# Performance work log

Measured on AMD Instinct MI355X. Metric: run time of the kernel, lower is better.

## Reference

```python
import jax, jax.numpy as jnp
import numpy as np

B, T, C = 256, 512, 256
K = 8  # number of distinct phoneme classes used (indices into phoneme_inventory)
# weights dict {'aa':2.0,'ae':0.5,'ah':1.5,'ao':1.2,'aw':0.8}, rest default 1.0,
# materialized as a dense per-class-index weight vector:
WEIGHTS = np.ones(K, dtype=np.float32)
WEIGHTS[:5] = [2.0, 0.5, 1.5, 1.2, 0.8]


def setup_inputs() -> dict:
    key = jax.random.key(0)
    k1, k2 = jax.random.split(key)
    embeddings = jax.random.normal(k1, (B, T, C), dtype=jnp.float32)
    phonemes = jax.random.randint(k2, (B, T), 0, K, dtype=jnp.int64)
    weights = jnp.asarray(WEIGHTS)
    return {"embeddings": embeddings, "phonemes": phonemes, "weights": weights}


def reference(embeddings, phonemes, weights):
    Bs, Ts, Cs = embeddings.shape
    # F.normalize(p=2, dim=-1) with eps=1e-12
    norm = jnp.linalg.norm(embeddings, axis=-1, keepdims=True)
    emb = embeddings / jnp.maximum(norm, 1e-12)
    # all-pairs cosine similarity per timestep: [T, B, B]
    exp_sim = jnp.exp(jnp.einsum('itc,jtc->tij', emb, emb))
    eye = jnp.eye(Bs, dtype=bool)  # [B, B]
    p = phonemes.T  # [T, B]
    pos = (p[:, :, None] == p[:, None, :]) & ~eye  # [T, B, B]
    num = jnp.where(pos, exp_sim, 0.0).sum(-1)          # [T, B]
    den = jnp.where(~eye, exp_sim, 0.0).sum(-1)          # [T, B]
    per_sample = -jnp.log(num / (den + 1e-6))            # [T, B]
    # segment-mean per (timestep, class), then weighted mean over present classes
    oh = jax.nn.one_hot(p, weights.shape[0], dtype=per_sample.dtype)  # [T, B, K]
    counts = oh.sum(1)                                   # [T, K]
    sums = jnp.einsum('tb,tbk->tk', per_sample, oh)      # [T, K]
    present = counts > 0
    class_mean = sums / jnp.maximum(counts, 1.0)
    loss_t = jnp.where(present, class_mean * weights, 0.0).sum(-1) / present.sum(-1)
    return loss_t.mean()
```

## Files before the change

### kernel.cpp

```cpp
#include <hip/hip_runtime.h>

#define Bn 256
#define Tn 512
#define Cn 256
#define Kn 8

typedef __attribute__((ext_vector_type(4))) float f32x4;

__global__ __launch_bounds__(256, 8)
void conv_k(const float* __restrict__ emb, unsigned char* __restrict__ ws) {
    const int gid = blockIdx.x * 256 + threadIdx.x;
    const int b   = gid & 31;
    const int idx = gid >> 5;
    const int row = idx >> 9;
    const int t   = idx & (Tn - 1);
    const float4* p = (const float4*)(emb + (size_t)idx * Cn) + 2 * b;
    const float4 v0 = p[0];
    const float4 v1 = p[1];
    float ss = v0.x*v0.x + v0.y*v0.y + v0.z*v0.z + v0.w*v0.w
             + v1.x*v1.x + v1.y*v1.y + v1.z*v1.z + v1.w*v1.w;
    #pragma unroll
    for (int m = 1; m <= 16; m <<= 1) ss += __shfl_xor(ss, m, 64);
    const float inv = rsqrtf(fmaxf(ss, 1e-24f));
    int lo = __builtin_amdgcn_cvt_pk_fp8_f32(v0.x * inv, v0.y * inv, 0, false);
    lo     = __builtin_amdgcn_cvt_pk_fp8_f32(v0.z * inv, v0.w * inv, lo, true);
    int hi = __builtin_amdgcn_cvt_pk_fp8_f32(v1.x * inv, v1.y * inv, 0, false);
    hi     = __builtin_amdgcn_cvt_pk_fp8_f32(v1.z * inv, v1.w * inv, hi, true);
    const int q = b & 3, kk = b >> 2, kp = kk >> 1;
    const int phys = ((((q << 2) + kp) ^ (row & 7)) << 4) + ((kk & 1) << 3);
    int2 pk; pk.x = lo; pk.y = hi;
    *(int2*)&ws[(size_t)t * 65536 + row * 256 + phys] = pk;
}

__global__ __launch_bounds__(512, 4)
void tcon_k(const unsigned char* __restrict__ ws,
            const int* __restrict__ phon,
            const float* __restrict__ wts,
            float* __restrict__ out) {
    __shared__ __align__(16) unsigned char Esh[Bn * Bn];
    __shared__ int   pcls[Bn];
    __shared__ float num_s[Bn], den_s[Bn];
    __shared__ float csum[Kn];
    __shared__ int   ccnt[Kn];

    const int t    = blockIdx.x;
    const int tid  = threadIdx.x;
    const int lane = tid & 63;
    const int wave = tid >> 6;

    if (tid < Kn) { csum[tid] = 0.0f; ccnt[tid] = 0; }
    if (tid < Bn) pcls[tid] = phon[tid * Tn + t];

    {
        const unsigned char* src = ws + (size_t)t * 65536;
        #pragma unroll
        for (int it = 0; it < 8; ++it) {
            const int off = it * 8192 + tid * 16;
            *(ulonglong2*)&Esh[off] = *(const ulonglong2*)&src[off];
        }
    }
    __syncthreads();

    const int q   = lane >> 4;
    const int l15 = lane & 15;
    const int e3  = l15 & 7;
    const int i0  = wave * 32;

    float num_p[8], den_p[8];
    int   pi[8];
    #pragma unroll
    for (int e = 0; e < 8; ++e) {
        const int irow = i0 + (e >> 2) * 16 + q * 4 + (e & 3);
        num_p[e] = 0.0f; den_p[e] = 0.0f;
        pi[e]    = pcls[irow];
    }

    f32x4 acc[2][4];
    for (int s = 0; s < 4; ++s) {
        const int jb = s * 64;
        #pragma unroll
        for (int m = 0; m < 2; ++m)
            #pragma unroll
            for (int n = 0; n < 4; ++n)
                acc[m][n] = (f32x4){0.f, 0.f, 0.f, 0.f};

        #pragma unroll
        for (int kp = 0; kp < 4; ++kp) {
            const int sw = (((q << 2) + kp) ^ e3) << 4;
            ulonglong2 a[2], bb[4];
            #pragma unroll
            for (int m = 0; m < 2; ++m)
                a[m] = *(const ulonglong2*)&Esh[(i0 + m * 16 + l15) * 256 + sw];
            #pragma unroll
            for (int n = 0; n < 4; ++n)
                bb[n] = *(const ulonglong2*)&Esh[(jb + n * 16 + l15) * 256 + sw];
            #pragma unroll
            for (int m = 0; m < 2; ++m)
                #pragma unroll
                for (int n = 0; n < 4; ++n) {
                    acc[m][n] = __builtin_amdgcn_mfma_f32_16x16x32_fp8_fp8(
                        (long)a[m].x, (long)bb[n].x, acc[m][n], 0, 0, 0);
                    acc[m][n] = __builtin_amdgcn_mfma_f32_16x16x32_fp8_fp8(
                        (long)a[m].y, (long)bb[n].y, acc[m][n], 0, 0, 0);
                }
        }

        #pragma unroll
        for (int n = 0; n < 4; ++n) {
            const int j  = jb + n * 16 + l15;
            const int pj = pcls[j];
            #pragma unroll
            for (int m = 0; m < 2; ++m)
                #pragma unroll
                for (int r = 0; r < 4; ++r) {
                    const int e  = m * 4 + r;
                    const int ir = i0 + m * 16 + q * 4 + r;
                    const float ex = __expf(acc[m][n][r]);
                    const bool nd = (ir != j);
                    den_p[e] += nd ? ex : 0.0f;
                    num_p[e] += (nd && (pj == pi[e])) ? ex : 0.0f;
                }
        }
    }

    #pragma unroll
    for (int e = 0; e < 8; ++e) {
        float n = num_p[e], d = den_p[e];
        #pragma unroll
        for (int m = 1; m <= 8; m <<= 1) {
            n += __shfl_xor(n, m, 64);
            d += __shfl_xor(d, m, 64);
        }
        if (l15 == e) {
            const int irow = i0 + (e >> 2) * 16 + q * 4 + (e & 3);
            num_s[irow] = n;
            den_s[irow] = d;
        }
    }
    __syncthreads();

    if (tid < Bn) {
        const float ps = __logf(den_s[tid] + 1e-6f) - __logf(num_s[tid]);
        atomicAdd(&csum[pcls[tid]], ps);
        atomicAdd(&ccnt[pcls[tid]], 1);
    }
    __syncthreads();

    if (tid == 0) {
        float accv = 0.0f; int np = 0;
        #pragma unroll
        for (int k = 0; k < Kn; ++k)
            if (ccnt[k] > 0) { accv += (csum[k] / (float)ccnt[k]) * wts[k]; ++np; }
        atomicAdd(out, (accv / (float)np) * (1.0f / (float)Tn));
    }
}

extern "C" void kernel_launch(void* const* d_in, const int* in_sizes, int n_in,
                              void* d_out, int out_size, void* d_ws, size_t ws_size,
                              hipStream_t stream) {
    const float* emb  = (const float*)d_in[0];
    const int*   phon = (const int*)d_in[1];
    const float* wts  = (const float*)d_in[2];
    float*       out  = (float*)d_out;
    unsigned char* ws = (unsigned char*)d_ws;

    hipMemsetAsync(out, 0, sizeof(float), stream);
    conv_k<<<(Bn * Tn * 32) / 256, 256, 0, stream>>>(emb, ws);
    tcon_k<<<Tn, 512, 0, stream>>>(ws, phon, wts, out);
}
```

Baseline: 216.5 us.

## Fuse normalization and FP8 conversion into the contrastive kernel, hoist A fragments

Removes the separate conversion kernel and its 8 MB FP8 workspace round-trip. Each block now reads its timestep's fp32 rows directly, normalizes them with a wave-wide shuffle reduction, and writes swizzled FP8 into shared memory. The A-operand fragments are also loaded once into registers instead of once per j-stage. The trade-off is that global reads now take one 1 KB row per wave-iteration, strided by T*C, which may cut achieved bandwidth, and the extra fragment registers raise register pressure.

```diff
diff --git a/kernel.cpp b/kernel.cpp
--- a/kernel.cpp
+++ b/kernel.cpp
@@ -7,33 +7,8 @@
 
 typedef __attribute__((ext_vector_type(4))) float f32x4;
 
-__global__ __launch_bounds__(256, 8)
-void conv_k(const float* __restrict__ emb, unsigned char* __restrict__ ws) {
-    const int gid = blockIdx.x * 256 + threadIdx.x;
-    const int b   = gid & 31;
-    const int idx = gid >> 5;
-    const int row = idx >> 9;
-    const int t   = idx & (Tn - 1);
-    const float4* p = (const float4*)(emb + (size_t)idx * Cn) + 2 * b;
-    const float4 v0 = p[0];
-    const float4 v1 = p[1];
-    float ss = v0.x*v0.x + v0.y*v0.y + v0.z*v0.z + v0.w*v0.w
-             + v1.x*v1.x + v1.y*v1.y + v1.z*v1.z + v1.w*v1.w;
-    #pragma unroll
-    for (int m = 1; m <= 16; m <<= 1) ss += __shfl_xor(ss, m, 64);
-    const float inv = rsqrtf(fmaxf(ss, 1e-24f));
-    int lo = __builtin_amdgcn_cvt_pk_fp8_f32(v0.x * inv, v0.y * inv, 0, false);
-    lo     = __builtin_amdgcn_cvt_pk_fp8_f32(v0.z * inv, v0.w * inv, lo, true);
-    int hi = __builtin_amdgcn_cvt_pk_fp8_f32(v1.x * inv, v1.y * inv, 0, false);
-    hi     = __builtin_amdgcn_cvt_pk_fp8_f32(v1.z * inv, v1.w * inv, hi, true);
-    const int q = b & 3, kk = b >> 2, kp = kk >> 1;
-    const int phys = ((((q << 2) + kp) ^ (row & 7)) << 4) + ((kk & 1) << 3);
-    int2 pk; pk.x = lo; pk.y = hi;
-    *(int2*)&ws[(size_t)t * 65536 + row * 256 + phys] = pk;
-}
-
 __global__ __launch_bounds__(512, 4)
-void tcon_k(const unsigned char* __restrict__ ws,
+void tcon_k(const float* __restrict__ emb,
             const int* __restrict__ phon,
             const float* __restrict__ wts,
             float* __restrict__ out) {
@@ -52,11 +27,21 @@
     if (tid < Bn) pcls[tid] = phon[tid * Tn + t];
 
     {
-        const unsigned char* src = ws + (size_t)t * 65536;
-        #pragma unroll
-        for (int it = 0; it < 8; ++it) {
-            const int off = it * 8192 + tid * 16;
-            *(ulonglong2*)&Esh[off] = *(const ulonglong2*)&src[off];
+        const int q8   = (lane >> 1) & 3;
+        const int kk8  = lane >> 3;
+        const int ubase = (q8 << 2) + (kk8 >> 1);
+        const int obase = ((kk8 & 1) << 3) + ((lane & 1) << 2);
+        #pragma unroll 4
+        for (int rr = 0; rr < 32; ++rr) {
+            const int row = wave * 32 + rr;
+            const float4 v = ((const float4*)(emb + ((size_t)row * Tn + t) * Cn))[lane];
+            float ss = v.x * v.x + v.y * v.y + v.z * v.z + v.w * v.w;
+            #pragma unroll
+            for (int m = 1; m <= 32; m <<= 1) ss += __shfl_xor(ss, m, 64);
+            const float inv = rsqrtf(fmaxf(ss, 1e-24f));
+            int pk = __builtin_amdgcn_cvt_pk_fp8_f32(v.x * inv, v.y * inv, 0, false);
+            pk     = __builtin_amdgcn_cvt_pk_fp8_f32(v.z * inv, v.w * inv, pk, true);
+            *(int*)&Esh[row * 256 + ((ubase ^ (row & 7)) << 4) + obase] = pk;
         }
     }
     __syncthreads();
@@ -75,6 +60,14 @@
         pi[e]    = pcls[irow];
     }
 
+    ulonglong2 afr[2][4];
+    #pragma unroll
+    for (int m = 0; m < 2; ++m)
+        #pragma unroll
+        for (int kp = 0; kp < 4; ++kp)
+            afr[m][kp] = *(const ulonglong2*)
+                &Esh[(i0 + m * 16 + l15) * 256 + ((((q << 2) + kp) ^ e3) << 4)];
+
     f32x4 acc[2][4];
     for (int s = 0; s < 4; ++s) {
         const int jb = s * 64;
@@ -87,10 +80,7 @@
         #pragma unroll
         for (int kp = 0; kp < 4; ++kp) {
             const int sw = (((q << 2) + kp) ^ e3) << 4;
-            ulonglong2 a[2], bb[4];
-            #pragma unroll
-            for (int m = 0; m < 2; ++m)
-                a[m] = *(const ulonglong2*)&Esh[(i0 + m * 16 + l15) * 256 + sw];
+            ulonglong2 bb[4];
             #pragma unroll
             for (int n = 0; n < 4; ++n)
                 bb[n] = *(const ulonglong2*)&Esh[(jb + n * 16 + l15) * 256 + sw];
@@ -99,9 +89,9 @@
                 #pragma unroll
                 for (int n = 0; n < 4; ++n) {
                     acc[m][n] = __builtin_amdgcn_mfma_f32_16x16x32_fp8_fp8(
-                        (long)a[m].x, (long)bb[n].x, acc[m][n], 0, 0, 0);
+                        (long)afr[m][kp].x, (long)bb[n].x, acc[m][n], 0, 0, 0);
                     acc[m][n] = __builtin_amdgcn_mfma_f32_16x16x32_fp8_fp8(
-                        (long)a[m].y, (long)bb[n].y, acc[m][n], 0, 0, 0);
+                        (long)afr[m][kp].y, (long)bb[n].y, acc[m][n], 0, 0, 0);
                 }
         }
 
@@ -162,9 +152,7 @@
     const int*   phon = (const int*)d_in[1];
     const float* wts  = (const float*)d_in[2];
     float*       out  = (float*)d_out;
-    unsigned char* ws = (unsigned char*)d_ws;
 
     hipMemsetAsync(out, 0, sizeof(float), stream);
-    conv_k<<<(Bn * Tn * 32) / 256, 256, 0, stream>>>(emb, ws);
-    tcon_k<<<Tn, 512, 0, stream>>>(ws, phon, wts, out);
+    tcon_k<<<Tn, 512, 0, stream>>>(emb, phon, wts, out);
 }
```

New measurement: 221.7 us. 1.02x slower.

## Fuse normalization and FP8 conversion into the contrastive kernel

Applied to the files above, without the earlier changes.

Removes the separate conversion kernel and its FP8 workspace. Each time-step block now loads its 256 fp32 rows directly from the embeddings, normalizes them, converts to FP8 and writes them straight into the swizzled shared-memory tile. This saves one launch and the workspace write and read-back. The cost is that each block reads rows with a stride of T*C floats, so global reads become scattered, and the conversion work now sits before the MFMA phase with no overlap.

```diff
diff --git a/kernel.cpp b/kernel.cpp
--- a/kernel.cpp
+++ b/kernel.cpp
@@ -7,33 +7,8 @@
 
 typedef __attribute__((ext_vector_type(4))) float f32x4;
 
-__global__ __launch_bounds__(256, 8)
-void conv_k(const float* __restrict__ emb, unsigned char* __restrict__ ws) {
-    const int gid = blockIdx.x * 256 + threadIdx.x;
-    const int b   = gid & 31;
-    const int idx = gid >> 5;
-    const int row = idx >> 9;
-    const int t   = idx & (Tn - 1);
-    const float4* p = (const float4*)(emb + (size_t)idx * Cn) + 2 * b;
-    const float4 v0 = p[0];
-    const float4 v1 = p[1];
-    float ss = v0.x*v0.x + v0.y*v0.y + v0.z*v0.z + v0.w*v0.w
-             + v1.x*v1.x + v1.y*v1.y + v1.z*v1.z + v1.w*v1.w;
-    #pragma unroll
-    for (int m = 1; m <= 16; m <<= 1) ss += __shfl_xor(ss, m, 64);
-    const float inv = rsqrtf(fmaxf(ss, 1e-24f));
-    int lo = __builtin_amdgcn_cvt_pk_fp8_f32(v0.x * inv, v0.y * inv, 0, false);
-    lo     = __builtin_amdgcn_cvt_pk_fp8_f32(v0.z * inv, v0.w * inv, lo, true);
-    int hi = __builtin_amdgcn_cvt_pk_fp8_f32(v1.x * inv, v1.y * inv, 0, false);
-    hi     = __builtin_amdgcn_cvt_pk_fp8_f32(v1.z * inv, v1.w * inv, hi, true);
-    const int q = b & 3, kk = b >> 2, kp = kk >> 1;
-    const int phys = ((((q << 2) + kp) ^ (row & 7)) << 4) + ((kk & 1) << 3);
-    int2 pk; pk.x = lo; pk.y = hi;
-    *(int2*)&ws[(size_t)t * 65536 + row * 256 + phys] = pk;
-}
-
 __global__ __launch_bounds__(512, 4)
-void tcon_k(const unsigned char* __restrict__ ws,
+void tcon_k(const float* __restrict__ emb,
             const int* __restrict__ phon,
             const float* __restrict__ wts,
             float* __restrict__ out) {
@@ -52,11 +27,28 @@
     if (tid < Bn) pcls[tid] = phon[tid * Tn + t];
 
     {
-        const unsigned char* src = ws + (size_t)t * 65536;
-        #pragma unroll
-        for (int it = 0; it < 8; ++it) {
-            const int off = it * 8192 + tid * 16;
-            *(ulonglong2*)&Esh[off] = *(const ulonglong2*)&src[off];
+        const int b     = lane & 31;
+        const int q     = b & 3;
+        const int kk    = b >> 2;
+        const int ubase = (q << 2) + (kk >> 1);
+        const int half8 = (kk & 1) << 3;
+        #pragma unroll 4
+        for (int it = 0; it < 16; ++it) {
+            const int row = wave * 2 + (lane >> 5) + it * 16;
+            const float4* p = (const float4*)(emb + ((size_t)row * Tn + t) * Cn) + 2 * b;
+            const float4 v0 = p[0];
+            const float4 v1 = p[1];
+            float ss = v0.x*v0.x + v0.y*v0.y + v0.z*v0.z + v0.w*v0.w
+                     + v1.x*v1.x + v1.y*v1.y + v1.z*v1.z + v1.w*v1.w;
+            #pragma unroll
+            for (int m = 1; m <= 16; m <<= 1) ss += __shfl_xor(ss, m, 64);
+            const float inv = rsqrtf(fmaxf(ss, 1e-24f));
+            int lo = __builtin_amdgcn_cvt_pk_fp8_f32(v0.x * inv, v0.y * inv, 0, false);
+            lo     = __builtin_amdgcn_cvt_pk_fp8_f32(v0.z * inv, v0.w * inv, lo, true);
+            int hi = __builtin_amdgcn_cvt_pk_fp8_f32(v1.x * inv, v1.y * inv, 0, false);
+            hi     = __builtin_amdgcn_cvt_pk_fp8_f32(v1.z * inv, v1.w * inv, hi, true);
+            int2 pk; pk.x = lo; pk.y = hi;
+            *(int2*)&Esh[row * 256 + ((ubase ^ (row & 7)) << 4) + half8] = pk;
         }
     }
     __syncthreads();
@@ -162,9 +154,7 @@
     const int*   phon = (const int*)d_in[1];
     const float* wts  = (const float*)d_in[2];
     float*       out  = (float*)d_out;
-    unsigned char* ws = (unsigned char*)d_ws;
 
     hipMemsetAsync(out, 0, sizeof(float), stream);
-    conv_k<<<(Bn * Tn * 32) / 256, 256, 0, stream>>>(emb, ws);
-    tcon_k<<<Tn, 512, 0, stream>>>(ws, phon, wts, out);
+    tcon_k<<<Tn, 512, 0, stream>>>(emb, phon, wts, out);
 }
```

Result: no change. 216.4 us (-0.0%).
